# Kernel tuning notes

Measured on AMD Instinct MI355X. Metric: run time of the kernel, lower is better.

Reference implementation:

```python
import jax, jax.numpy as jnp
import numpy as np

N, M = 4096, 8192
IN_DIM, OUT_DIM = 4096, 1024
NUM_SAMPLE = 10


def setup_inputs() -> dict:
    key = jax.random.key(0)
    k1, k2, k3, k4, k5 = jax.random.split(key, 5)
    node_features = jax.random.normal(k1, (N, IN_DIM), dtype=jnp.float32)
    neighbor_features = jax.random.normal(k2, (M, IN_DIM), dtype=jnp.float32)
    # Xavier-ish scale for params
    weight = jax.random.normal(k3, (OUT_DIM, IN_DIM), dtype=jnp.float32) * (1.0 / np.sqrt(IN_DIM))
    attention_vector = jax.random.normal(k4, (2 * OUT_DIM, 1), dtype=jnp.float32) * 0.05
    neighbor_idx = jax.random.randint(k5, (N, NUM_SAMPLE), 0, M, dtype=jnp.int32)
    return {
        "node_features": node_features,
        "neighbor_features": neighbor_features,
        "weight": weight,
        "attention_vector": attention_vector,
        "neighbor_idx": neighbor_idx,
    }


def reference(node_features, neighbor_features, weight, attention_vector, neighbor_idx):
    # Linear transform: [N, out], [M, out]
    node_t = node_features @ weight.T
    neigh_t = neighbor_features @ weight.T

    # combined @ attention_vector decomposes:
    # cat([h_i, h_j]) @ a == h_i @ a1 + h_j @ a2  (same math, no [N,M,2*out] tensor)
    a1 = attention_vector[:OUT_DIM, 0]   # [out]
    a2 = attention_vector[OUT_DIM:, 0]   # [out]
    scores = jax.nn.leaky_relu((node_t @ a1)[:, None] + (neigh_t @ a2)[None, :],
                               negative_slope=0.2)  # [N, M]

    # Build dense 0/1 mask from sampled neighbor indices (ragged -> dense)
    rows = jnp.arange(N, dtype=jnp.int32)[:, None]                  # [N,1]
    mask = jnp.zeros((N, M), dtype=jnp.float32).at[rows, neighbor_idx].set(1.0)

    scores = jnp.where(mask == 0, -jnp.inf, scores)
    attn = jax.nn.softmax(scores, axis=1)           # masked softmax over neighbor pool
    return attn @ neigh_t                           # [N, out]
```

## Files before the change

kernel.cpp:

```cpp
#include <hip/hip_runtime.h>

#define IN_DIM  4096
#define OUT_DIM 1024
#define NN      4096
#define MM      8192
#define NSAMP   10

typedef __bf16 bf16x8 __attribute__((ext_vector_type(8)));
typedef float  fx4    __attribute__((ext_vector_type(4)));

__device__ __forceinline__ ushort f2bf(float f) {
    union { float f; unsigned u; } v; v.f = f;
    unsigned u = v.u;
    return (ushort)((u + 0x7FFFu + ((u >> 16) & 1u)) >> 16);
}

#define GLDS(g, l) __builtin_amdgcn_global_load_lds(                           \
    (const __attribute__((address_space(1))) unsigned*)(g),                    \
    (__attribute__((address_space(3))) unsigned*)(l), 16, 0, 0)

__global__ __launch_bounds__(256) void k_attvec(const float* __restrict__ W,
                                                const float* __restrict__ att,
                                                float* __restrict__ v1,
                                                float* __restrict__ v2,
                                                ushort* __restrict__ Wbf) {
    int k  = blockIdx.x * 256 + threadIdx.x;
    int o0 = blockIdx.y * 128;
    float s1 = 0.f, s2 = 0.f;
    for (int o = o0; o < o0 + 128; ++o) {
        float w = W[(size_t)o * IN_DIM + k];
        Wbf[(size_t)o * IN_DIM + k] = f2bf(w);
        s1 += att[o] * w;
        s2 += att[OUT_DIM + o] * w;
    }
    atomicAdd(&v1[k], s1);
    atomicAdd(&v2[k], s2);
}

__global__ __launch_bounds__(256) void k_node_alpha(const float* __restrict__ X,
                                                    const float* __restrict__ v1,
                                                    float* __restrict__ outv) {
    int row = blockIdx.x;
    const float4* xr = reinterpret_cast<const float4*>(X + (size_t)row * IN_DIM);
    const float4* vr = reinterpret_cast<const float4*>(v1);
    float s = 0.f;
    for (int i = threadIdx.x; i < IN_DIM / 4; i += 256) {
        float4 a = xr[i], b = vr[i];
        s += a.x * b.x + a.y * b.y + a.z * b.z + a.w * b.w;
    }
    for (int off = 32; off > 0; off >>= 1) s += __shfl_down(s, off, 64);
    __shared__ float ws[4];
    if ((threadIdx.x & 63) == 0) ws[threadIdx.x >> 6] = s;
    __syncthreads();
    if (threadIdx.x == 0) outv[row] = ws[0] + ws[1] + ws[2] + ws[3];
}

__global__ __launch_bounds__(256) void k_cast_beta(const float* __restrict__ X,
                                                   const float* __restrict__ v2,
                                                   ushort* __restrict__ Xbf,
                                                   float* __restrict__ beta) {
    int row = blockIdx.x;
    const float4* xr = reinterpret_cast<const float4*>(X + (size_t)row * IN_DIM);
    const float4* vr = reinterpret_cast<const float4*>(v2);
    ushort4* yr = reinterpret_cast<ushort4*>(Xbf + (size_t)row * IN_DIM);
    float s = 0.f;
    for (int i = threadIdx.x; i < IN_DIM / 4; i += 256) {
        float4 a = xr[i], b = vr[i];
        s += a.x * b.x + a.y * b.y + a.z * b.z + a.w * b.w;
        ushort4 o;
        o.x = f2bf(a.x); o.y = f2bf(a.y); o.z = f2bf(a.z); o.w = f2bf(a.w);
        yr[i] = o;
    }
    for (int off = 32; off > 0; off >>= 1) s += __shfl_down(s, off, 64);
    __shared__ float ws[4];
    if ((threadIdx.x & 63) == 0) ws[threadIdx.x >> 6] = s;
    __syncthreads();
    if (threadIdx.x == 0) beta[row] = ws[0] + ws[1] + ws[2] + ws[3];
}

#define TM 128
#define TN 128
#define BK 32

__global__ __launch_bounds__(256) void k_gemm(const ushort* __restrict__ A,
                                              const ushort* __restrict__ B,
                                              float* __restrict__ C) {
    __shared__ __align__(16) ushort As[TM * BK];
    __shared__ __align__(16) ushort Bs[TN * BK];
    const int tid  = threadIdx.x;
    const int lane = tid & 63;
    const int wave = tid >> 6;
    const int wm   = (wave >> 1) * 64;
    const int wn   = (wave & 1) * 64;
    const int bm   = blockIdx.x * TM;
    const int bn   = blockIdx.y * TN;
    const int quad = lane >> 4;
    const int lrow = lane & 15;

    const int srow  = wave * 32 + (lane >> 2);
    const int skoff = (lane & 3) * 8;
    const ushort* gA = A + (size_t)(bm + srow) * IN_DIM + skoff;
    const ushort* gB = B + (size_t)(bn + srow) * IN_DIM + skoff;
    ushort* lA = As + wave * 1024;
    ushort* lB = Bs + wave * 1024;

    fx4 acc[4][4] = {};

    for (int k0 = 0; k0 < IN_DIM; k0 += BK) {
        GLDS(gA + k0,                lA);
        GLDS(gA + k0 + 16 * IN_DIM,  lA + 512);
        GLDS(gB + k0,                lB);
        GLDS(gB + k0 + 16 * IN_DIM,  lB + 512);
        __syncthreads();

        bf16x8 af[4], bfr[4];
#pragma unroll
        for (int mi = 0; mi < 4; ++mi)
            af[mi] = *reinterpret_cast<const bf16x8*>(As + (wm + mi * 16 + lrow) * BK + quad * 8);
#pragma unroll
        for (int ni = 0; ni < 4; ++ni)
            bfr[ni] = *reinterpret_cast<const bf16x8*>(Bs + (wn + ni * 16 + lrow) * BK + quad * 8);
#pragma unroll
        for (int mi = 0; mi < 4; ++mi)
#pragma unroll
            for (int ni = 0; ni < 4; ++ni)
                acc[mi][ni] = __builtin_amdgcn_mfma_f32_16x16x32_bf16(af[mi], bfr[ni], acc[mi][ni], 0, 0, 0);
        __syncthreads();
    }

#pragma unroll
    for (int mi = 0; mi < 4; ++mi)
#pragma unroll
        for (int ni = 0; ni < 4; ++ni) {
            int r = bm + wm + mi * 16 + quad * 4;
            int c = bn + wn + ni * 16 + lrow;
#pragma unroll
            for (int v = 0; v < 4; ++v)
                C[(size_t)(r + v) * OUT_DIM + c] = acc[mi][ni][v];
        }
}

__global__ __launch_bounds__(256) void k_aggregate(const float* __restrict__ neigh_t,
                                                   const float* __restrict__ nalpha,
                                                   const float* __restrict__ nbeta,
                                                   const int* __restrict__ nidx,
                                                   float* __restrict__ outp) {
    int row = blockIdx.x;
    __shared__ int   s_idx[NSAMP];
    __shared__ float s_w[NSAMP];
    __shared__ int   s_cnt;
    if (threadIdx.x == 0) {
        int   tmp[NSAMP];
        float sc[NSAMP];
        int   cnt = 0;
        float alpha = nalpha[row];
        float mx = -INFINITY;
        for (int s = 0; s < NSAMP; ++s) {
            int j = nidx[row * NSAMP + s];
            bool dup = false;
            for (int t = 0; t < cnt; ++t)
                if (tmp[t] == j) { dup = true; break; }
            if (!dup) {
                float x = alpha + nbeta[j];
                float v = x > 0.f ? x : 0.2f * x;
                tmp[cnt] = j;
                sc[cnt] = v;
                if (v > mx) mx = v;
                ++cnt;
            }
        }
        float sum = 0.f;
        for (int t = 0; t < cnt; ++t) { float e = expf(sc[t] - mx); sc[t] = e; sum += e; }
        float inv = 1.f / sum;
        for (int t = 0; t < cnt; ++t) { s_idx[t] = tmp[t]; s_w[t] = sc[t] * inv; }
        s_cnt = cnt;
    }
    __syncthreads();
    int cnt = s_cnt;
    int col = threadIdx.x * 4;
    float ax = 0.f, ay = 0.f, az = 0.f, aw = 0.f;
    for (int t = 0; t < cnt; ++t) {
        float w = s_w[t];
        float4 v = *reinterpret_cast<const float4*>(neigh_t + (size_t)s_idx[t] * OUT_DIM + col);
        ax += w * v.x; ay += w * v.y; az += w * v.z; aw += w * v.w;
    }
    float4 o; o.x = ax; o.y = ay; o.z = az; o.w = aw;
    *reinterpret_cast<float4*>(outp + (size_t)row * OUT_DIM + col) = o;
}

extern "C" void kernel_launch(void* const* d_in, const int* in_sizes, int n_in,
                              void* d_out, int out_size, void* d_ws, size_t ws_size,
                              hipStream_t stream) {
    const float* node_f  = (const float*)d_in[0];
    const float* neigh_f = (const float*)d_in[1];
    const float* W       = (const float*)d_in[2];
    const float* att     = (const float*)d_in[3];
    const int*   nidx    = (const int*)d_in[4];
    float* outp = (float*)d_out;

    char* ws = (char*)d_ws;
    ushort* Abf     = (ushort*)ws;
    ushort* Wbf     = (ushort*)(ws + 67108864);
    float*  neigh_t = (float*)(ws + 75497472);
    float*  v1      = (float*)(ws + 109051904);
    float*  v2      = v1 + IN_DIM;
    float*  nalpha  = v2 + IN_DIM;
    float*  nbeta   = nalpha + NN;

    hipMemsetAsync(v1, 0, 2 * IN_DIM * sizeof(float), stream);

    k_attvec    <<<dim3(16, 8), 256, 0, stream>>>(W, att, v1, v2, Wbf);
    k_node_alpha<<<NN,          256, 0, stream>>>(node_f, v1, nalpha);
    k_cast_beta <<<MM,          256, 0, stream>>>(neigh_f, v2, Abf, nbeta);
    k_gemm      <<<dim3(MM / TM, OUT_DIM / TN), 256, 0, stream>>>(Abf, Wbf, neigh_t);
    k_aggregate <<<NN,          256, 0, stream>>>(neigh_t, nalpha, nbeta, nidx, outp);
}
```

Before: 438.9 us.

## Split GEMM K dimension in two with bf16 partials summed in aggregate

The neighbor GEMM now splits its K loop across two z-blocks, doubling the grid from 512 to 1024 blocks to improve CU occupancy. Each half writes its partial result as bf16 into a separate buffer, and the aggregation kernel loads both partials and adds them. This halves the output write size per partial and removes a separate reduction pass, but rounds the partial sums to bf16, which costs accuracy. It also adds a launch-bounds occupancy hint.

```diff
diff --git a/kernel.cpp b/kernel.cpp
--- a/kernel.cpp
+++ b/kernel.cpp
@@ -13,6 +13,10 @@
     union { float f; unsigned u; } v; v.f = f;
     unsigned u = v.u;
     return (ushort)((u + 0x7FFFu + ((u >> 16) & 1u)) >> 16);
+}
+__device__ __forceinline__ float bf2f(ushort u) {
+    union { unsigned u; float f; } v; v.u = ((unsigned)u) << 16;
+    return v.f;
 }
 
 #define GLDS(g, l) __builtin_amdgcn_global_load_lds(                           \
@@ -81,10 +85,11 @@
 #define TM 128
 #define TN 128
 #define BK 32
-
-__global__ __launch_bounds__(256) void k_gemm(const ushort* __restrict__ A,
-                                              const ushort* __restrict__ B,
-                                              float* __restrict__ C) {
+#define KSPLIT (IN_DIM / 2)
+
+__global__ __launch_bounds__(256, 4) void k_gemm(const ushort* __restrict__ A,
+                                                 const ushort* __restrict__ B,
+                                                 ushort* __restrict__ P) {
     __shared__ __align__(16) ushort As[TM * BK];
     __shared__ __align__(16) ushort Bs[TN * BK];
     const int tid  = threadIdx.x;
@@ -94,19 +99,20 @@
     const int wn   = (wave & 1) * 64;
     const int bm   = blockIdx.x * TM;
     const int bn   = blockIdx.y * TN;
+    const int kb   = blockIdx.z * KSPLIT;
     const int quad = lane >> 4;
     const int lrow = lane & 15;
 
     const int srow  = wave * 32 + (lane >> 2);
     const int skoff = (lane & 3) * 8;
-    const ushort* gA = A + (size_t)(bm + srow) * IN_DIM + skoff;
-    const ushort* gB = B + (size_t)(bn + srow) * IN_DIM + skoff;
+    const ushort* gA = A + (size_t)(bm + srow) * IN_DIM + kb + skoff;
+    const ushort* gB = B + (size_t)(bn + srow) * IN_DIM + kb + skoff;
     ushort* lA = As + wave * 1024;
     ushort* lB = Bs + wave * 1024;
 
     fx4 acc[4][4] = {};
 
-    for (int k0 = 0; k0 < IN_DIM; k0 += BK) {
+    for (int k0 = 0; k0 < KSPLIT; k0 += BK) {
         GLDS(gA + k0,                lA);
         GLDS(gA + k0 + 16 * IN_DIM,  lA + 512);
         GLDS(gB + k0,                lB);
@@ -128,6 +134,7 @@
         __syncthreads();
     }
 
+    ushort* Pz = P + (size_t)blockIdx.z * MM * OUT_DIM;
 #pragma unroll
     for (int mi = 0; mi < 4; ++mi)
 #pragma unroll
@@ -136,11 +143,11 @@
             int c = bn + wn + ni * 16 + lrow;
 #pragma unroll
             for (int v = 0; v < 4; ++v)
-                C[(size_t)(r + v) * OUT_DIM + c] = acc[mi][ni][v];
+                Pz[(size_t)(r + v) * OUT_DIM + c] = f2bf(acc[mi][ni][v]);
         }
 }
 
-__global__ __launch_bounds__(256) void k_aggregate(const float* __restrict__ neigh_t,
+__global__ __launch_bounds__(256) void k_aggregate(const ushort* __restrict__ P,
                                                    const float* __restrict__ nalpha,
                                                    const float* __restrict__ nbeta,
                                                    const int* __restrict__ nidx,
@@ -181,8 +188,13 @@
     float ax = 0.f, ay = 0.f, az = 0.f, aw = 0.f;
     for (int t = 0; t < cnt; ++t) {
         float w = s_w[t];
-        float4 v = *reinterpret_cast<const float4*>(neigh_t + (size_t)s_idx[t] * OUT_DIM + col);
-        ax += w * v.x; ay += w * v.y; az += w * v.z; aw += w * v.w;
+        size_t off = (size_t)s_idx[t] * OUT_DIM + col;
+        ushort4 u0 = *reinterpret_cast<const ushort4*>(P + off);
+        ushort4 u1 = *reinterpret_cast<const ushort4*>(P + (size_t)MM * OUT_DIM + off);
+        ax += w * (bf2f(u0.x) + bf2f(u1.x));
+        ay += w * (bf2f(u0.y) + bf2f(u1.y));
+        az += w * (bf2f(u0.z) + bf2f(u1.z));
+        aw += w * (bf2f(u0.w) + bf2f(u1.w));
     }
     float4 o; o.x = ax; o.y = ay; o.z = az; o.w = aw;
     *reinterpret_cast<float4*>(outp + (size_t)row * OUT_DIM + col) = o;
@@ -199,19 +211,19 @@
     float* outp = (float*)d_out;
 
     char* ws = (char*)d_ws;
-    ushort* Abf     = (ushort*)ws;
-    ushort* Wbf     = (ushort*)(ws + 67108864);
-    float*  neigh_t = (float*)(ws + 75497472);
-    float*  v1      = (float*)(ws + 109051904);
-    float*  v2      = v1 + IN_DIM;
-    float*  nalpha  = v2 + IN_DIM;
-    float*  nbeta   = nalpha + NN;
+    ushort* Abf = (ushort*)ws;
+    ushort* Wbf = (ushort*)(ws + 67108864);
+    ushort* P   = (ushort*)(ws + 75497472);
+    float*  v1     = (float*)(ws + 109051904);
+    float*  v2     = v1 + IN_DIM;
+    float*  nalpha = v2 + IN_DIM;
+    float*  nbeta  = nalpha + NN;
 
     hipMemsetAsync(v1, 0, 2 * IN_DIM * sizeof(float), stream);
 
     k_attvec    <<<dim3(16, 8), 256, 0, stream>>>(W, att, v1, v2, Wbf);
     k_node_alpha<<<NN,          256, 0, stream>>>(node_f, v1, nalpha);
     k_cast_beta <<<MM,          256, 0, stream>>>(neigh_f, v2, Abf, nbeta);
-    k_gemm      <<<dim3(MM / TM, OUT_DIM / TN), 256, 0, stream>>>(Abf, Wbf, neigh_t);
-    k_aggregate <<<NN,          256, 0, stream>>>(neigh_t, nalpha, nbeta, nidx, outp);
-}
+    k_gemm      <<<dim3(MM / TM, OUT_DIM / TN, 2), 256, 0, stream>>>(Abf, Wbf, P);
+    k_aggregate <<<NN,          256, 0, stream>>>(P, nalpha, nbeta, nidx, outp);
+}
```

Result: faster. 398.9 us (-9.1%).
